# Performance work log

Hardware: AMD Instinct MI355X
Metric: run time of the kernel (lower is better)

The kernel has to match this reference:

```python
import jax, jax.numpy as jnp
import numpy as np

N_NODES = 100000
N_RELS = 237
N_EDGES = 500000
D_IN = 128
D_HID = 128
D_OUT = 128


def setup_inputs() -> dict:
    key = jax.random.key(0)
    ks = jax.random.split(key, 13)
    src = jax.random.randint(ks[0], (N_EDGES,), 0, N_NODES, dtype=jnp.int32)
    dst = jax.random.randint(ks[1], (N_EDGES,), 0, N_NODES, dtype=jnp.int32)
    rel = jax.random.randint(ks[2], (N_EDGES,), 0, N_RELS, dtype=jnp.int32)
    triplets = jnp.stack([src, dst, rel], axis=1)  # [E, 3]
    s = 0.05
    return {
        "triplets": triplets,
        "ent_embed": jax.random.normal(ks[3], (N_NODES, D_IN), jnp.float32) * s,
        "rel_embed": jax.random.normal(ks[4], (N_RELS, D_IN), jnp.float32) * s,
        "W_ent": jax.random.normal(ks[5], (D_IN, D_HID), jnp.float32) * s,
        "b_ent": jnp.zeros((D_HID,), jnp.float32),
        "W_rel": jax.random.normal(ks[6], (D_IN, D_HID), jnp.float32) * s,
        "b_rel": jnp.zeros((D_HID,), jnp.float32),
        "W_ent2": jax.random.normal(ks[7], (3 * D_HID, D_OUT), jnp.float32) * s,
        "b_ent2": jnp.zeros((D_OUT,), jnp.float32),
        "a_w": jax.random.normal(ks[8], (D_OUT, 1), jnp.float32) * s,
        "a_b": jnp.zeros((1,), jnp.float32),
    }


def reference(triplets, ent_embed, rel_embed, W_ent, b_ent, W_rel, b_rel,
              W_ent2, b_ent2, a_w, a_b):
    src_i, dst_i, rel_i = triplets[:, 0], triplets[:, 1], triplets[:, 2]
    # embedding gathers
    src = ent_embed[src_i]          # [E, D_IN]
    dst = ent_embed[dst_i]          # [E, D_IN]
    rel = rel_embed[rel_i]          # [E, D_IN]
    # shared fc_ent projection on src and dst, fc_rel on rel
    src = src @ W_ent + b_ent       # [E, D_HID]
    dst = dst @ W_ent + b_ent
    rel = rel @ W_rel + b_rel
    # per-edge feature c = fc_ent2(cat([src, dst, rel]))
    c = jnp.concatenate([src, dst, rel], axis=1) @ W_ent2 + b_ent2  # [E, D_OUT]
    # unnormalized exp attention score (leaky_relu slope 0.01, torch default)
    b = jnp.exp(jax.nn.leaky_relu((c @ a_w + a_b)[:, 0], negative_slope=0.01))  # [E]
    # segment softmax over edges sharing a source node
    b_sum = jax.ops.segment_sum(b, src_i, num_segments=N_NODES)  # [N]
    alpha = b / b_sum[src_i]                                     # [E]
    # weighted neighbor aggregation per source node
    h = jax.ops.segment_sum(alpha[:, None] * c, src_i, num_segments=N_NODES)  # [N, D_OUT]
    return h
```

## Files before the change

### kernel.cpp

```cpp
#include <hip/hip_runtime.h>
#include <hip/hip_bf16.h>

#define N_NODES_C 100000
#define N_PAD_C   100096
#define N_RELS_C  237
#define N_EDGES_C 500000
#define D 128

#define NBLK_GEMM 782
#define NBLK_REL  60
#define NBLK_HIST 128

typedef __attribute__((ext_vector_type(8))) short short8;
typedef __attribute__((ext_vector_type(4))) float f32x4;

__device__ __forceinline__ ushort f2bf(float x) {
    union { float f; uint u; } v; v.f = x;
    uint r = v.u + 0x7FFFu + ((v.u >> 16) & 1u);
    return (ushort)(r >> 16);
}
__device__ __forceinline__ float bf2f_hi(uint u) {
    union { uint u; float f; } v; v.u = u; return v.f;
}

__global__ void k_fuse_w(const float* __restrict__ W_ent, const float* __restrict__ W_rel,
                         const float* __restrict__ W_ent2,
                         const float* __restrict__ b_ent, const float* __restrict__ b_rel,
                         const float* __restrict__ b_ent2,
                         const float* __restrict__ a_w, const float* __restrict__ a_b,
                         float* __restrict__ WR, ushort* __restrict__ WfTb,
                         float* __restrict__ biasC, float* __restrict__ sConst,
                         int* __restrict__ deg) {
    int j = threadIdx.x;
    int k = blockIdx.x;
    int which = blockIdx.y;
    if (which == 0) {
        float acc = 0.f;
        for (int i = 0; i < D; ++i) acc += W_ent[k*D+i] * W_ent2[i*D+j];
        WfTb[j*D + k] = f2bf(acc);
    } else if (which == 1) {
        float acc = 0.f;
        for (int i = 0; i < D; ++i) acc += W_ent[k*D+i] * W_ent2[(D+i)*D+j];
        WfTb[(D+j)*D + k] = f2bf(acc);
    } else if (which == 2) {
        float acc = 0.f;
        for (int i = 0; i < D; ++i) acc += W_rel[k*D+i] * W_ent2[(2*D+i)*D+j];
        WR[k*D + j] = acc;
    } else if (k == 0) {
        __shared__ float red[128];
        float acc = b_ent2[j];
        for (int i = 0; i < D; ++i) {
            acc += b_ent[i] * (W_ent2[i*D+j] + W_ent2[(D+i)*D+j]);
            acc += b_rel[i] * W_ent2[(2*D+i)*D+j];
        }
        biasC[j] = acc;
        red[j] = acc * a_w[j];
        __syncthreads();
        for (int s = 64; s > 0; s >>= 1) { if (j < s) red[j] += red[j+s]; __syncthreads(); }
        if (j == 0) sConst[0] = red[0] + a_b[0];
    } else {
        int idx = (k - 1) * 128 + j;
        for (int i = idx; i < N_NODES_C; i += 127 * 128) deg[i] = 0;
    }
}

__global__ __launch_bounds__(512, 4) void k1_mega(const float* __restrict__ ent,
                                                  const ushort* __restrict__ WfTb,
                                                  const float* __restrict__ a_w,
                                                  const float* __restrict__ relE,
                                                  const float* __restrict__ WR,
                                                  const int* __restrict__ trip,
                                                  ushort* __restrict__ AnB,
                                                  ushort* __restrict__ BnB,
                                                  ushort* __restrict__ RmB,
                                                  float* __restrict__ sA,
                                                  float* __restrict__ sB,
                                                  float* __restrict__ sR,
                                                  int* __restrict__ deg,
                                                  int n_nodes) {
    __shared__ __align__(16) ushort wL[256*128];
    int tid = threadIdx.x;
    int blk = blockIdx.x;

    if (blk >= NBLK_GEMM + NBLK_REL) {
        int hb = blk - NBLK_GEMM - NBLK_REL;
        for (int e = hb*512 + tid; e < N_EDGES_C; e += NBLK_HIST*512) {
            int s = trip[3*e];
            if ((unsigned)s < (unsigned)N_NODES_C) atomicAdd(&deg[s], 1);
        }
        return;
    }
    if (blk >= NBLK_GEMM) {
        __shared__ float red[512];
        int sub = tid >> 7, j = tid & 127;
        int r = (blk - NBLK_GEMM)*4 + sub;
        float acc = 0.f;
        if (r < N_RELS_C) {
            for (int k = 0; k < D; ++k) acc += relE[r*D+k] * WR[k*D+j];
            RmB[r*D + j] = f2bf(acc);
        }
        red[tid] = acc * a_w[j];
        __syncthreads();
        for (int s = 64; s > 0; s >>= 1) {
            if (j < s) red[sub*128 + j] += red[sub*128 + j + s];
            __syncthreads();
        }
        if (j == 0 && r < N_RELS_C) sR[r] = red[sub*128];
        return;
    }

    int m0 = blk * 128;
#pragma unroll
    for (int u = 0; u < 8; ++u) {
        int f = u*512 + tid;
        int r = f >> 4, k16 = f & 15;
        *(uint4*)&wL[r*128 + ((k16 ^ (r & 15)) << 3)] =
            *(const uint4*)&WfTb[r*128 + (k16 << 3)];
    }
    __syncthreads();

    int wave = tid >> 6, lane = tid & 63;
    int ny = wave >> 2;
    int q = lane >> 4, c = lane & 15;
    int wm = (wave & 3) * 32;

    f32x4 acc[2][8];
#pragma unroll
    for (int mt = 0; mt < 2; ++mt)
#pragma unroll
        for (int nt = 0; nt < 8; ++nt) { f32x4 z = {0.f,0.f,0.f,0.f}; acc[mt][nt] = z; }

#pragma unroll
    for (int chunk = 0; chunk < 4; ++chunk) {
        int k16 = chunk*4 + q;
        short8 a[2];
#pragma unroll
        for (int mt = 0; mt < 2; ++mt) {
            int row = m0 + wm + mt*16 + c;
            float4 e0 = make_float4(0.f,0.f,0.f,0.f), e1 = e0;
            if (row < n_nodes) {
                const float* ep = &ent[(size_t)row*D + (k16 << 3)];
                e0 = *(const float4*)ep;
                e1 = *(const float4*)(ep + 4);
            }
            short8 pk;
            pk[0]=(short)f2bf(e0.x); pk[1]=(short)f2bf(e0.y); pk[2]=(short)f2bf(e0.z); pk[3]=(short)f2bf(e0.w);
            pk[4]=(short)f2bf(e1.x); pk[5]=(short)f2bf(e1.y); pk[6]=(short)f2bf(e1.z); pk[7]=(short)f2bf(e1.w);
            a[mt] = pk;
        }
#pragma unroll
        for (int nt = 0; nt < 8; ++nt) {
            int wrow = ny*128 + nt*16 + c;
            short8 b = *(const short8*)&wL[wrow*128 + ((k16 ^ c) << 3)];
            acc[0][nt] = __builtin_amdgcn_mfma_f32_16x16x32_bf16(a[0], b, acc[0][nt], 0, 0, 0);
            acc[1][nt] = __builtin_amdgcn_mfma_f32_16x16x32_bf16(a[1], b, acc[1][nt], 0, 0, 0);
        }
    }

    float aw[8];
#pragma unroll
    for (int nt = 0; nt < 8; ++nt) aw[nt] = a_w[nt*16 + c];

    ushort* out  = ny ? BnB : AnB;
    float*  sOut = ny ? sB  : sA;

#pragma unroll
    for (int mt = 0; mt < 2; ++mt) {
#pragma unroll
        for (int reg = 0; reg < 4; ++reg) {
            int m = m0 + wm + mt*16 + q*4 + reg;
            float pa = 0.f;
#pragma unroll
            for (int nt = 0; nt < 8; ++nt) pa += acc[mt][nt][reg] * aw[nt];
#pragma unroll
            for (int msk = 1; msk < 16; msk <<= 1) pa += __shfl_xor(pa, msk);
            if (m < n_nodes) {
                if (c == 0) sOut[m] = pa;
#pragma unroll
                for (int nt = 0; nt < 8; ++nt)
                    out[(size_t)m*D + nt*16 + c] = f2bf(acc[mt][nt][reg]);
            }
        }
    }
}

__global__ void k_scan1(const int* __restrict__ deg, int* __restrict__ off,
                        int* __restrict__ bsum, int n) {
    __shared__ int s[1024];
    int i = blockIdx.x*1024 + threadIdx.x;
    int v = (i < n) ? deg[i] : 0;
    s[threadIdx.x] = v; __syncthreads();
    for (int d = 1; d < 1024; d <<= 1) {
        int t = (threadIdx.x >= d) ? s[threadIdx.x - d] : 0;
        __syncthreads();
        s[threadIdx.x] += t;
        __syncthreads();
    }
    if (i < n) off[i] = s[threadIdx.x] - v;
    if (threadIdx.x == 1023) bsum[blockIdx.x] = s[1023];
}

__global__ void k_scan23(int* __restrict__ off, int* __restrict__ cursor,
                         const int* __restrict__ bsum, int n, int nb, int total_edges) {
    __shared__ int s[128];
    int t = threadIdx.x;
    if (t < 128) s[t] = (t < nb) ? bsum[t] : 0;
    __syncthreads();
    for (int d = 1; d < 128; d <<= 1) {
        int u = (t < 128 && t >= d) ? s[t - d] : 0;
        __syncthreads();
        if (t < 128) s[t] += u;
        __syncthreads();
    }
    int add = (blockIdx.x > 0) ? s[blockIdx.x - 1] : 0;
    int i = blockIdx.x*1024 + t;
    if (i < n) {
        int o = off[i] + add;
        off[i] = o;
        cursor[i] = o;
    }
    if (i == 0) off[n] = total_edges;
}

__global__ void k_edge_b(const int* __restrict__ trip, const float* __restrict__ sB,
                         const float* __restrict__ sR, int* __restrict__ cursor,
                         uint2* __restrict__ kb, int n_edges) {
    int e = blockIdx.x*256 + threadIdx.x;
    if (e >= n_edges) return;
    int s = trip[3*e], d = trip[3*e+1], r = trip[3*e+2];
    if ((unsigned)s >= (unsigned)N_NODES_C || (unsigned)d >= (unsigned)N_NODES_C ||
        (unsigned)r >= (unsigned)N_RELS_C) return;
    float v = sB[d] + sR[r];
    int p = atomicAdd(&cursor[s], 1);
    kb[p] = make_uint2((uint)(d | (r << 20)), __float_as_uint(v));
}

__global__ void k_aggregate(const int* __restrict__ off, const uint2* __restrict__ kb,
                            const ushort* __restrict__ AnB, const ushort* __restrict__ BnB,
                            const ushort* __restrict__ RmB, const float* __restrict__ biasC,
                            const float* __restrict__ sA, const float* __restrict__ sConst,
                            float* __restrict__ h, int n_nodes) {
    int g = threadIdx.x >> 4, lane = threadIdx.x & 15;
    int n = blockIdx.x*16 + g;
    if (n >= n_nodes) return;
    int o0 = off[n], o1 = off[n+1];
    int c = lane*8;
    float* hp = &h[(size_t)n*D + c];
    if (o0 == o1) {
        *(float4*)hp     = make_float4(0.f,0.f,0.f,0.f);
        *(float4*)(hp+4) = make_float4(0.f,0.f,0.f,0.f);
        return;
    }
    float t = sA[n] + sConst[0];
    float num[8];
#pragma unroll
    for (int i = 0; i < 8; ++i) num[i] = 0.f;
    float den = 0.f;

    for (int p = o0; p < o1; p += 4) {
        uint2 kv[4]; uint4 gB[4], gR[4]; float vmask[4];
#pragma unroll
        for (int u = 0; u < 4; ++u) {
            int q = p + u;
            vmask[u] = (q < o1) ? 1.f : 0.f;
            int pc = (q < o1) ? q : (o1 - 1);
            kv[u] = kb[pc];
        }
#pragma unroll
        for (int u = 0; u < 4; ++u) {
            gB[u] = *(const uint4*)&BnB[(size_t)(kv[u].x & 0xFFFFF)*D + c];
            gR[u] = *(const uint4*)&RmB[(size_t)(kv[u].x >> 20)*D + c];
        }
#pragma unroll
        for (int u = 0; u < 4; ++u) {
            float logit = t + __uint_as_float(kv[u].y);
            float l = logit > 0.f ? logit : 0.01f*logit;
            float b = vmask[u] * expf(l);
            den += b;
            const uint* bu = (const uint*)&gB[u];
            const uint* ru = (const uint*)&gR[u];
#pragma unroll
            for (int i = 0; i < 4; ++i) {
                num[2*i]   += b * (bf2f_hi(bu[i] << 16)         + bf2f_hi(ru[i] << 16));
                num[2*i+1] += b * (bf2f_hi(bu[i] & 0xFFFF0000u) + bf2f_hi(ru[i] & 0xFFFF0000u));
            }
        }
    }

    float inv = 1.f / den;
    uint4 araw = *(const uint4*)&AnB[(size_t)n*D + c];
    const uint* au = (const uint*)&araw;
    float4 bc0 = *(const float4*)&biasC[c];
    float4 bc1 = *(const float4*)&biasC[c+4];
    float4 o0v, o1v;
    o0v.x = bf2f_hi(au[0] << 16)         + bc0.x + num[0]*inv;
    o0v.y = bf2f_hi(au[0] & 0xFFFF0000u) + bc0.y + num[1]*inv;
    o0v.z = bf2f_hi(au[1] << 16)         + bc0.z + num[2]*inv;
    o0v.w = bf2f_hi(au[1] & 0xFFFF0000u) + bc0.w + num[3]*inv;
    o1v.x = bf2f_hi(au[2] << 16)         + bc1.x + num[4]*inv;
    o1v.y = bf2f_hi(au[2] & 0xFFFF0000u) + bc1.y + num[5]*inv;
    o1v.z = bf2f_hi(au[3] << 16)         + bc1.z + num[6]*inv;
    o1v.w = bf2f_hi(au[3] & 0xFFFF0000u) + bc1.w + num[7]*inv;
    *(float4*)hp     = o0v;
    *(float4*)(hp+4) = o1v;
}

extern "C" void kernel_launch(void* const* d_in, const int* in_sizes, int n_in,
                              void* d_out, int out_size, void* d_ws, size_t ws_size,
                              hipStream_t stream) {
    const int*   trip   = (const int*)  d_in[0];
    const float* ent    = (const float*)d_in[1];
    const float* relE   = (const float*)d_in[2];
    const float* W_ent  = (const float*)d_in[3];
    const float* b_ent  = (const float*)d_in[4];
    const float* W_rel  = (const float*)d_in[5];
    const float* b_rel  = (const float*)d_in[6];
    const float* W_ent2 = (const float*)d_in[7];
    const float* b_ent2 = (const float*)d_in[8];
    const float* a_w    = (const float*)d_in[9];
    const float* a_b    = (const float*)d_in[10];
    float* h = (float*)d_out;

    char* ws = (char*)d_ws;
    size_t o = 0;
    auto alloc = [&](size_t bytes) { size_t p = o; o += (bytes + 255) & ~(size_t)255; return p; };
    float*  WR     = (float*) (ws + alloc(128*128*4));
    ushort* WfTb   = (ushort*)(ws + alloc(256*128*2));
    float*  biasC  = (float*) (ws + alloc(128*4));
    ushort* RmB    = (ushort*)(ws + alloc((size_t)N_RELS_C*128*2));
    float*  sR     = (float*) (ws + alloc(N_RELS_C*4));
    float*  sConst = (float*) (ws + alloc(4));
    float*  sA     = (float*) (ws + alloc((size_t)N_NODES_C*4));
    float*  sB     = (float*) (ws + alloc((size_t)N_NODES_C*4));
    int*    deg    = (int*)   (ws + alloc((size_t)N_NODES_C*4));
    int*    off    = (int*)   (ws + alloc(((size_t)N_NODES_C+1)*4));
    int*    cursor = (int*)   (ws + alloc((size_t)N_NODES_C*4));
    int*    bsum   = (int*)   (ws + alloc(128*4));
    uint2*  kb     = (uint2*) (ws + alloc((size_t)N_EDGES_C*8));
    ushort* BnB    = (ushort*)(ws + alloc((size_t)N_PAD_C*128*2));
    ushort* AnB    = (ushort*)(ws + alloc((size_t)N_PAD_C*128*2));

    k_fuse_w<<<dim3(128,4), 128, 0, stream>>>(W_ent, W_rel, W_ent2, b_ent, b_rel, b_ent2,
                                              a_w, a_b, WR, WfTb, biasC, sConst, deg);
    k1_mega<<<NBLK_GEMM + NBLK_REL + NBLK_HIST, 512, 0, stream>>>(
        ent, WfTb, a_w, relE, WR, trip, AnB, BnB, RmB, sA, sB, sR, deg, N_NODES_C);
    int nb = (N_NODES_C + 1023)/1024;
    k_scan1<<<nb, 1024, 0, stream>>>(deg, off, bsum, N_NODES_C);
    k_scan23<<<nb, 1024, 0, stream>>>(off, cursor, bsum, N_NODES_C, nb, N_EDGES_C);
    k_edge_b<<<(N_EDGES_C+255)/256, 256, 0, stream>>>(trip, sB, sR, cursor, kb, N_EDGES_C);
    k_aggregate<<<(N_NODES_C+15)/16, 256, 0, stream>>>(off, kb, AnB, BnB, RmB, biasC,
                                                       sA, sConst, h, N_NODES_C);
}
```

Baseline: 227.4 us.

## Split node GEMM blocks by output half and reorder block roles in mega kernel

Each GEMM block now computes only one 128-column half (A or B projection), so shared memory holds a 128x128 weight slice instead of 256x128 and the grid doubles to 1564 GEMM blocks. Launch bounds rise from 4 to 6 blocks per SM. The entity-row loads are issued before the weight copy to overlap latency, and the histogram and relation blocks are moved to the front of the grid so they start first. The cost is that each entity row is now read and converted to bf16 twice, once per half, raising global read traffic.

Measured after the change: 224.1 us. No clear change (-1.5%).

```diff
diff --git a/kernel.cpp b/kernel.cpp
--- a/kernel.cpp
+++ b/kernel.cpp
@@ -7,9 +7,10 @@
 #define N_EDGES_C 500000
 #define D 128
 
-#define NBLK_GEMM 782
+#define NBLK_HIST 128
 #define NBLK_REL  60
-#define NBLK_HIST 128
+#define NBLK_GEMM 1564
+#define GEMM0     (NBLK_HIST + NBLK_REL)
 
 typedef __attribute__((ext_vector_type(8))) short short8;
 typedef __attribute__((ext_vector_type(4))) float f32x4;
@@ -64,7 +65,7 @@
     }
 }
 
-__global__ __launch_bounds__(512, 4) void k1_mega(const float* __restrict__ ent,
+__global__ __launch_bounds__(512, 6) void k1_mega(const float* __restrict__ ent,
                                                   const ushort* __restrict__ WfTb,
                                                   const float* __restrict__ a_w,
                                                   const float* __restrict__ relE,
@@ -78,22 +79,21 @@
                                                   float* __restrict__ sR,
                                                   int* __restrict__ deg,
                                                   int n_nodes) {
-    __shared__ __align__(16) ushort wL[256*128];
+    __shared__ __align__(16) ushort wL[128*128];
     int tid = threadIdx.x;
     int blk = blockIdx.x;
 
-    if (blk >= NBLK_GEMM + NBLK_REL) {
-        int hb = blk - NBLK_GEMM - NBLK_REL;
-        for (int e = hb*512 + tid; e < N_EDGES_C; e += NBLK_HIST*512) {
+    if (blk < NBLK_HIST) {
+        for (int e = blk*512 + tid; e < N_EDGES_C; e += NBLK_HIST*512) {
             int s = trip[3*e];
             if ((unsigned)s < (unsigned)N_NODES_C) atomicAdd(&deg[s], 1);
         }
         return;
     }
-    if (blk >= NBLK_GEMM) {
+    if (blk < GEMM0) {
         __shared__ float red[512];
         int sub = tid >> 7, j = tid & 127;
-        int r = (blk - NBLK_GEMM)*4 + sub;
+        int r = (blk - NBLK_HIST)*4 + sub;
         float acc = 0.f;
         if (r < N_RELS_C) {
             for (int k = 0; k < D; ++k) acc += relE[r*D+k] * WR[k*D+j];
@@ -109,51 +109,63 @@
         return;
     }
 
-    int m0 = blk * 128;
-#pragma unroll
-    for (int u = 0; u < 8; ++u) {
+    int g    = blk - GEMM0;
+    int tile = g >> 1;
+    int half = g & 1;
+    int m0   = tile * 128;
+
+    int wave = tid >> 6, lane = tid & 63;
+    int q = lane >> 4, c = lane & 15;
+
+    int row = m0 + wave*16 + c;
+    float4 e0[4], e1[4];
+#pragma unroll
+    for (int chunk = 0; chunk < 4; ++chunk) {
+        e0[chunk] = make_float4(0.f,0.f,0.f,0.f);
+        e1[chunk] = e0[chunk];
+    }
+    if (row < n_nodes) {
+        const float* ep = &ent[(size_t)row*D];
+#pragma unroll
+        for (int chunk = 0; chunk < 4; ++chunk) {
+            int k16 = chunk*4 + q;
+            e0[chunk] = *(const float4*)(ep + (k16 << 3));
+            e1[chunk] = *(const float4*)(ep + (k16 << 3) + 4);
+        }
+    }
+
+#pragma unroll
+    for (int u = 0; u < 4; ++u) {
         int f = u*512 + tid;
         int r = f >> 4, k16 = f & 15;
         *(uint4*)&wL[r*128 + ((k16 ^ (r & 15)) << 3)] =
-            *(const uint4*)&WfTb[r*128 + (k16 << 3)];
+            *(const uint4*)&WfTb[(half*128 + r)*128 + (k16 << 3)];
+    }
+
+    short8 a[4];
+#pragma unroll
+    for (int chunk = 0; chunk < 4; ++chunk) {
+        short8 pk;
+        pk[0]=(short)f2bf(e0[chunk].x); pk[1]=(short)f2bf(e0[chunk].y);
+        pk[2]=(short)f2bf(e0[chunk].z); pk[3]=(short)f2bf(e0[chunk].w);
+        pk[4]=(short)f2bf(e1[chunk].x); pk[5]=(short)f2bf(e1[chunk].y);
+        pk[6]=(short)f2bf(e1[chunk].z); pk[7]=(short)f2bf(e1[chunk].w);
+        a[chunk] = pk;
     }
     __syncthreads();
 
-    int wave = tid >> 6, lane = tid & 63;
-    int ny = wave >> 2;
-    int q = lane >> 4, c = lane & 15;
-    int wm = (wave & 3) * 32;
-
-    f32x4 acc[2][8];
-#pragma unroll
-    for (int mt = 0; mt < 2; ++mt)
-#pragma unroll
-        for (int nt = 0; nt < 8; ++nt) { f32x4 z = {0.f,0.f,0.f,0.f}; acc[mt][nt] = z; }
+    f32x4 acc[8];
+#pragma unroll
+    for (int nt = 0; nt < 8; ++nt) { f32x4 z = {0.f,0.f,0.f,0.f}; acc[nt] = z; }
 
 #pragma unroll
     for (int chunk = 0; chunk < 4; ++chunk) {
         int k16 = chunk*4 + q;
-        short8 a[2];
-#pragma unroll
-        for (int mt = 0; mt < 2; ++mt) {
-            int row = m0 + wm + mt*16 + c;
-            float4 e0 = make_float4(0.f,0.f,0.f,0.f), e1 = e0;
-            if (row < n_nodes) {
-                const float* ep = &ent[(size_t)row*D + (k16 << 3)];
-                e0 = *(const float4*)ep;
-                e1 = *(const float4*)(ep + 4);
-            }
-            short8 pk;
-            pk[0]=(short)f2bf(e0.x); pk[1]=(short)f2bf(e0.y); pk[2]=(short)f2bf(e0.z); pk[3]=(short)f2bf(e0.w);
-            pk[4]=(short)f2bf(e1.x); pk[5]=(short)f2bf(e1.y); pk[6]=(short)f2bf(e1.z); pk[7]=(short)f2bf(e1.w);
-            a[mt] = pk;
-        }
 #pragma unroll
         for (int nt = 0; nt < 8; ++nt) {
-            int wrow = ny*128 + nt*16 + c;
+            int wrow = nt*16 + c;
             short8 b = *(const short8*)&wL[wrow*128 + ((k16 ^ c) << 3)];
-            acc[0][nt] = __builtin_amdgcn_mfma_f32_16x16x32_bf16(a[0], b, acc[0][nt], 0, 0, 0);
-            acc[1][nt] = __builtin_amdgcn_mfma_f32_16x16x32_bf16(a[1], b, acc[1][nt], 0, 0, 0);
+            acc[nt] = __builtin_amdgcn_mfma_f32_16x16x32_bf16(a[chunk], b, acc[nt], 0, 0, 0);
         }
     }
 
@@ -161,25 +173,22 @@
 #pragma unroll
     for (int nt = 0; nt < 8; ++nt) aw[nt] = a_w[nt*16 + c];
 
-    ushort* out  = ny ? BnB : AnB;
-    float*  sOut = ny ? sB  : sA;
-
-#pragma unroll
-    for (int mt = 0; mt < 2; ++mt) {
-#pragma unroll
-        for (int reg = 0; reg < 4; ++reg) {
-            int m = m0 + wm + mt*16 + q*4 + reg;
-            float pa = 0.f;
-#pragma unroll
-            for (int nt = 0; nt < 8; ++nt) pa += acc[mt][nt][reg] * aw[nt];
-#pragma unroll
-            for (int msk = 1; msk < 16; msk <<= 1) pa += __shfl_xor(pa, msk);
-            if (m < n_nodes) {
-                if (c == 0) sOut[m] = pa;
-#pragma unroll
-                for (int nt = 0; nt < 8; ++nt)
-                    out[(size_t)m*D + nt*16 + c] = f2bf(acc[mt][nt][reg]);
-            }
+    ushort* out  = half ? BnB : AnB;
+    float*  sOut = half ? sB  : sA;
+
+#pragma unroll
+    for (int reg = 0; reg < 4; ++reg) {
+        int m = m0 + wave*16 + q*4 + reg;
+        float pa = 0.f;
+#pragma unroll
+        for (int nt = 0; nt < 8; ++nt) pa += acc[nt][reg] * aw[nt];
+#pragma unroll
+        for (int msk = 1; msk < 16; msk <<= 1) pa += __shfl_xor(pa, msk);
+        if (m < n_nodes) {
+            if (c == 0) sOut[m] = pa;
+#pragma unroll
+            for (int nt = 0; nt < 8; ++nt)
+                out[(size_t)m*D + nt*16 + c] = f2bf(acc[nt][reg]);
         }
     }
 }
@@ -342,7 +351,7 @@
 
     k_fuse_w<<<dim3(128,4), 128, 0, stream>>>(W_ent, W_rel, W_ent2, b_ent, b_rel, b_ent2,
                                               a_w, a_b, WR, WfTb, biasC, sConst, deg);
-    k1_mega<<<NBLK_GEMM + NBLK_REL + NBLK_HIST, 512, 0, stream>>>(
+    k1_mega<<<GEMM0 + NBLK_GEMM, 512, 0, stream>>>(
         ent, WfTb, a_w, relE, WR, trip, AnB, BnB, RmB, sA, sB, sR, deg, N_NODES_C);
     int nb = (N_NODES_C + 1023)/1024;
     k_scan1<<<nb, 1024, 0, stream>>>(deg, off, bsum, N_NODES_C);
```
